# Kernel tuning notes

Measured on AMD Instinct MI355X. Metric: run time of the kernel, lower is better.

Reference implementation:

```python
import jax, jax.numpy as jnp
import numpy as np

ALPHA = 0.12
BETA = 0.88
OMEGA = 6.0
PHI_BASE = 0.0
B, T, D = 4, 4096, 2048


def setup_inputs() -> dict:
    key = jax.random.key(0)
    k1, = jax.random.split(key, 1)
    x = jax.random.normal(k1, (B, T, D), dtype=jnp.float32)
    gate = jnp.asarray(-2.0, dtype=jnp.float32)          # nn.Parameter gate_init
    input_scale = jnp.asarray(4.0, dtype=jnp.float32)     # nn.Parameter init 4.0
    mem_state = jnp.zeros((1, 1, D), dtype=jnp.float32)   # persistent buffer
    return {"x": x, "gate": gate, "input_scale": input_scale,
            "mem_state": mem_state, "step_idx": 0}


def reference(x, gate, input_scale, mem_state, step_idx):
    Bn, Tn, Dn = x.shape
    dtype = x.dtype
    # EMA recurrence: m_t = beta * m_{t-1} + alpha * input_scale * x_t
    u = (ALPHA * input_scale) * x                         # [B,T,D]
    m0 = jnp.broadcast_to(mem_state[:, 0, :], (Bn, Dn))   # [B,D]

    def step(m, u_t):
        m = BETA * m + u_t
        return m, m

    _, ms = jax.lax.scan(step, m0, jnp.swapaxes(u, 0, 1))  # [T,B,D]
    ms = jnp.swapaxes(ms, 0, 1)                            # [B,T,D]

    # log-periodic phase rotation per step (scalar angle per t)
    t_glob = jnp.arange(1, Tn + 1, dtype=dtype) + jnp.asarray(step_idx, dtype)
    theta = (OMEGA * jnp.log1p(t_glob) + PHI_BASE) % (2.0 * jnp.pi)  # [T]
    c = jnp.cos(theta)[None, :, None]
    s = jnp.sin(theta)[None, :, None]
    half = Dn // 2  # D even -> no tail
    a = ms[..., :half]
    b = ms[..., half:2 * half]
    m_rot = jnp.concatenate([a * c - b * s, a * s + b * c], axis=-1)  # [B,T,D]

    # residual gated output: y = x + sigmoid(gate) * m_seq
    return x + jax.nn.sigmoid(gate) * m_rot
```

## Files before the change

### kernel.cpp

```cpp
#include <hip/hip_runtime.h>
#include <math.h>

#define ALPHA 0.12f
#define BETA  0.88f
#define OMEGA 6.0f
#define TWO_PI 6.28318530717958647692f

constexpr int Bn   = 4;
constexpr int Tn   = 4096;
constexpr int Dn   = 2048;
constexpr int HALF = Dn / 2;
constexpr int L    = 64;
constexpr int NC   = Tn / L;

typedef float fx4 __attribute__((ext_vector_type(4)));

constexpr float beta_pow(int n) {
    float r = 1.0f;
    for (int i = 0; i < n; ++i) r *= BETA;
    return r;
}
constexpr float BETA_L = beta_pow(L);

__global__ void k_chunksum(const float* __restrict__ x,
                           const float* __restrict__ input_scale,
                           float* __restrict__ S) {
    int gid = blockIdx.x * blockDim.x + threadIdx.x;
    int d4 = gid & (Dn / 4 - 1);
    int c  = (gid >> 9) & (NC - 1);
    int b  = gid >> 15;
    const float sc = ALPHA * (*input_scale);

    const fx4* xp = (const fx4*)(x + ((size_t)b * Tn + (size_t)c * L) * Dn) + d4;
    fx4 m = (fx4)(0.0f);
#pragma unroll 8
    for (int i = 0; i < L; ++i) {
        fx4 v = xp[(size_t)i * (Dn / 4)];
        m = BETA * m + sc * v;
    }
    ((fx4*)S)[gid] = m;
}

__global__ void k_mid(float* __restrict__ SC,
                      const float* __restrict__ mem_state,
                      float* __restrict__ ctab, float* __restrict__ stab,
                      const int* __restrict__ step_idx) {
    if (blockIdx.x < 8) {
        int gid = blockIdx.x * blockDim.x + threadIdx.x;
        int d4 = gid & (Dn / 4 - 1);
        int b  = gid >> 9;
        fx4 m = ((const fx4*)mem_state)[d4];
        fx4* scp = (fx4*)SC;
        for (int c = 0; c < NC; ++c) {
            int idx = (b * NC + c) * (Dn / 4) + d4;
            fx4 s = scp[idx];
            scp[idx] = m;
            m = BETA_L * m + s;
        }
    } else {
        int t = (blockIdx.x - 8) * blockDim.x + threadIdx.x;
        float tg = (float)(t + 1 + *step_idx);
        float theta = fmodf(OMEGA * log1pf(tg), TWO_PI);
        ctab[t] = cosf(theta);
        stab[t] = sinf(theta);
    }
}

__global__ void k_final(const float* __restrict__ x,
                        const float* __restrict__ gate,
                        const float* __restrict__ input_scale,
                        const float* __restrict__ ctab,
                        const float* __restrict__ stab,
                        const float* __restrict__ C,
                        float* __restrict__ out) {
    int gid = blockIdx.x * blockDim.x + threadIdx.x;
    int p4 = gid & (HALF / 4 - 1);
    int c  = (gid >> 8) & (NC - 1);
    int b  = gid >> 14;

    const float sc  = ALPHA * (*input_scale);
    const float sig = 1.0f / (1.0f + expf(-(*gate)));

    size_t base = ((size_t)b * Tn + (size_t)c * L) * Dn;
    const fx4* xa = (const fx4*)(x + base) + p4;
    const fx4* xb = (const fx4*)(x + base + HALF) + p4;
    fx4* oa = (fx4*)(out + base) + p4;
    fx4* ob = (fx4*)(out + base + HALF) + p4;

    size_t cbase = (size_t)(b * NC + c) * Dn;
    fx4 ma = ((const fx4*)(C + cbase))[p4];
    fx4 mb = ((const fx4*)(C + cbase + HALF))[p4];

    int t0 = c * L;
#pragma unroll 4
    for (int i = 0; i < L; ++i) {
        fx4 va = xa[(size_t)i * (Dn / 4)];
        fx4 vb = xb[(size_t)i * (Dn / 4)];
        ma = BETA * ma + sc * va;
        mb = BETA * mb + sc * vb;
        float cth = ctab[t0 + i];
        float sth = stab[t0 + i];
        fx4 ra = va + sig * (ma * cth - mb * sth);
        fx4 rb = vb + sig * (ma * sth + mb * cth);
        __builtin_nontemporal_store(ra, &oa[(size_t)i * (Dn / 4)]);
        __builtin_nontemporal_store(rb, &ob[(size_t)i * (Dn / 4)]);
    }
}

extern "C" void kernel_launch(void* const* d_in, const int* in_sizes, int n_in,
                              void* d_out, int out_size, void* d_ws, size_t ws_size,
                              hipStream_t stream) {
    const float* x           = (const float*)d_in[0];
    const float* gate        = (const float*)d_in[1];
    const float* input_scale = (const float*)d_in[2];
    const float* mem_state   = (const float*)d_in[3];
    const int*   step_idx    = (const int*)d_in[4];
    float* out = (float*)d_out;

    float* ws   = (float*)d_ws;
    float* ctab = ws;
    float* stab = ws + Tn;
    float* SC   = ws + 2 * Tn;

    k_chunksum<<<(Bn * NC * Dn / 4) / 256, 256, 0, stream>>>(x, input_scale, SC);
    k_mid<<<8 + Tn / 256, 256, 0, stream>>>(SC, mem_state, ctab, stab, step_idx);
    k_final<<<(Bn * NC * HALF / 4) / 256, 256, 0, stream>>>(x, gate, input_scale,
                                                            ctab, stab, SC, out);
}
```

Before: 261.0 us.

## Drop the serial chunk-scan kernel by recomputing carry-ins inside the final kernel

Removes the middle kernel that ran a serial scan over 64 chunk sums using only 8 blocks. The cos/sin table computation moves into extra blocks of the chunk-sum kernel. Each block of the final kernel now rebuilds its own carry-in by folding the preceding chunk sums with beta^L, starting from mem_state. This saves one launch and the low-parallelism serial pass, at the cost of redundant reads of the chunk sums, up to 63 per block, mostly served from cache.

```diff
diff --git a/kernel.cpp b/kernel.cpp
--- a/kernel.cpp
+++ b/kernel.cpp
@@ -24,7 +24,17 @@
 
 __global__ void k_chunksum(const float* __restrict__ x,
                            const float* __restrict__ input_scale,
-                           float* __restrict__ S) {
+                           float* __restrict__ S,
+                           float* __restrict__ ctab, float* __restrict__ stab,
+                           const int* __restrict__ step_idx) {
+    if (blockIdx.x >= 512) {
+        int t = (blockIdx.x - 512) * blockDim.x + threadIdx.x;
+        float tg = (float)(t + 1 + *step_idx);
+        float theta = fmodf(OMEGA * log1pf(tg), TWO_PI);
+        ctab[t] = cosf(theta);
+        stab[t] = sinf(theta);
+        return;
+    }
     int gid = blockIdx.x * blockDim.x + threadIdx.x;
     int d4 = gid & (Dn / 4 - 1);
     int c  = (gid >> 9) & (NC - 1);
@@ -41,55 +51,36 @@
     ((fx4*)S)[gid] = m;
 }
 
-__global__ void k_mid(float* __restrict__ SC,
-                      const float* __restrict__ mem_state,
-                      float* __restrict__ ctab, float* __restrict__ stab,
-                      const int* __restrict__ step_idx) {
-    if (blockIdx.x < 8) {
-        int gid = blockIdx.x * blockDim.x + threadIdx.x;
-        int d4 = gid & (Dn / 4 - 1);
-        int b  = gid >> 9;
-        fx4 m = ((const fx4*)mem_state)[d4];
-        fx4* scp = (fx4*)SC;
-        for (int c = 0; c < NC; ++c) {
-            int idx = (b * NC + c) * (Dn / 4) + d4;
-            fx4 s = scp[idx];
-            scp[idx] = m;
-            m = BETA_L * m + s;
-        }
-    } else {
-        int t = (blockIdx.x - 8) * blockDim.x + threadIdx.x;
-        float tg = (float)(t + 1 + *step_idx);
-        float theta = fmodf(OMEGA * log1pf(tg), TWO_PI);
-        ctab[t] = cosf(theta);
-        stab[t] = sinf(theta);
-    }
-}
-
 __global__ void k_final(const float* __restrict__ x,
                         const float* __restrict__ gate,
                         const float* __restrict__ input_scale,
                         const float* __restrict__ ctab,
                         const float* __restrict__ stab,
-                        const float* __restrict__ C,
+                        const float* __restrict__ S,
+                        const float* __restrict__ mem_state,
                         float* __restrict__ out) {
-    int gid = blockIdx.x * blockDim.x + threadIdx.x;
-    int p4 = gid & (HALF / 4 - 1);
-    int c  = (gid >> 8) & (NC - 1);
-    int b  = gid >> 14;
+    int p4 = threadIdx.x;
+    int c  = blockIdx.x & (NC - 1);
+    int b  = blockIdx.x >> 6;
 
     const float sc  = ALPHA * (*input_scale);
     const float sig = 1.0f / (1.0f + expf(-(*gate)));
+
+    fx4 ma = ((const fx4*)mem_state)[p4];
+    fx4 mb = ((const fx4*)mem_state)[p4 + HALF / 4];
+    const fx4* Sa = (const fx4*)(S + (size_t)b * NC * Dn) + p4;
+    const fx4* Sb = (const fx4*)(S + (size_t)b * NC * Dn + HALF) + p4;
+#pragma unroll 4
+    for (int j = 0; j < c; ++j) {
+        ma = BETA_L * ma + Sa[(size_t)j * (Dn / 4)];
+        mb = BETA_L * mb + Sb[(size_t)j * (Dn / 4)];
+    }
 
     size_t base = ((size_t)b * Tn + (size_t)c * L) * Dn;
     const fx4* xa = (const fx4*)(x + base) + p4;
     const fx4* xb = (const fx4*)(x + base + HALF) + p4;
     fx4* oa = (fx4*)(out + base) + p4;
     fx4* ob = (fx4*)(out + base + HALF) + p4;
-
-    size_t cbase = (size_t)(b * NC + c) * Dn;
-    fx4 ma = ((const fx4*)(C + cbase))[p4];
-    fx4 mb = ((const fx4*)(C + cbase + HALF))[p4];
 
     int t0 = c * L;
 #pragma unroll 4
@@ -122,8 +113,8 @@
     float* stab = ws + Tn;
     float* SC   = ws + 2 * Tn;
 
-    k_chunksum<<<(Bn * NC * Dn / 4) / 256, 256, 0, stream>>>(x, input_scale, SC);
-    k_mid<<<8 + Tn / 256, 256, 0, stream>>>(SC, mem_state, ctab, stab, step_idx);
-    k_final<<<(Bn * NC * HALF / 4) / 256, 256, 0, stream>>>(x, gate, input_scale,
-                                                            ctab, stab, SC, out);
+    k_chunksum<<<512 + Tn / 256, 256, 0, stream>>>(x, input_scale, SC,
+                                                   ctab, stab, step_idx);
+    k_final<<<Bn * NC, 256, 0, stream>>>(x, gate, input_scale, ctab, stab,
+                                         SC, mem_state, out);
 }
```

New measurement: 258.0 us. No clear change (-1.2%).
